# Optimization experiments

Hardware: AMD Instinct MI355X
Metric: run time of the kernel (lower is better)

## Reference

```python
import jax, jax.numpy as jnp
import numpy as np

B, N, FEAT, HID, CTX = 16384, 7, 512, 256, 256
COMB = N * HID + CTX  # 2048


def setup_inputs() -> dict:
    key = jax.random.key(0)
    ks = jax.random.split(key, 20)
    s = lambda k, shape, sc=0.05: jax.random.normal(k, shape, dtype=jnp.float32) * sc
    adj = jax.random.randint(ks[1], (N, N), 0, 2).astype(jnp.float32)
    # guarantee self-loops so no row is fully masked (still exercise nan_to_num path robustly)
    adj = jnp.maximum(adj, jnp.eye(N, dtype=jnp.float32))
    return {
        "node_feats": jax.random.normal(ks[0], (B, N, FEAT), dtype=jnp.float32),
        "adj": adj,
        "context": jax.random.normal(ks[2], (B, CTX), dtype=jnp.float32),
        "base_preds": jax.random.normal(ks[3], (B, 5), dtype=jnp.float32),
        "W1": s(ks[4], (HID, FEAT)),
        "a1": s(ks[5], (1, 2 * HID)),
        "W2": s(ks[6], (HID, HID)),
        "a2": s(ks[7], (1, 2 * HID)),
        "wh1_w": s(ks[8], (32, COMB)), "wh1_b": s(ks[9], (32,)),
        "wh2_w": s(ks[10], (16, 32)), "wh2_b": s(ks[11], (16,)),
        "wh3_w": s(ks[12], (5, 16)), "wh3_b": s(ks[13], (5,)),
        "rh1_w": s(ks[14], (16, COMB)), "rh1_b": s(ks[15], (16,)),
        "rh2_w": s(ks[16], (1, 16)), "rh2_b": s(ks[17], (1,)),
    }


def _gat_layer(x, adj, W, a):
    # x: (B, N, in_dim); W: (D, in_dim); a: (1, 2D)
    h = jnp.einsum('bni,di->bnd', x, W)  # (B, N, D)
    D = W.shape[0]
    # a([h_i, h_j]) == h_i @ a[:, :D] + h_j @ a[:, D:]
    s_i = h @ a[0, :D]   # (B, N)
    s_j = h @ a[0, D:]   # (B, N)
    e = s_i[:, :, None] + s_j[:, None, :]          # (B, N, N)
    e = jax.nn.leaky_relu(e, negative_slope=0.2)
    e = jnp.where(adj[None] == 0, -jnp.inf, e)
    alpha = jax.nn.softmax(e, axis=-1)
    alpha = jnp.nan_to_num(alpha, nan=0.0)
    out = jnp.einsum('bij,bjd->bid', alpha, h)     # (B, N, D)
    return out, alpha


def reference(node_feats, adj, context, base_preds, W1, a1, W2, a2,
              wh1_w, wh1_b, wh2_w, wh2_b, wh3_w, wh3_b,
              rh1_w, rh1_b, rh2_w, rh2_b):
    h, _attn1 = _gat_layer(node_feats, adj, W1, a1)
    h = jax.nn.relu(h)
    h, attn2 = _gat_layer(h, adj, W2, a2)
    h = jax.nn.relu(h)
    graph_embed = h.reshape(h.shape[0], -1)                 # (B, N*D)
    combined = jnp.concatenate([graph_embed, context], -1)  # (B, COMB)
    # weight head (dropout is inference-mode identity)
    t = jax.nn.relu(combined @ wh1_w.T + wh1_b)
    t = jax.nn.relu(t @ wh2_w.T + wh2_b)
    raw_weights = t @ wh3_w.T + wh3_b                       # (B, 5)
    weights = jax.nn.softmax(raw_weights, axis=-1)
    weighted_pred = jnp.sum(weights * base_preds, axis=-1)  # (B,)
    r = jnp.tanh(combined @ rh1_w.T + rh1_b)
    residual = (r @ rh2_w.T + rh2_b)[:, 0] * 0.05
    pred = jnp.maximum(weighted_pred + residual, 0.05)
    return pred, weights, attn2
```

## Files before the change

### kernel.cpp

```cpp
#include <hip/hip_runtime.h>

#define B_SZ 16384
#define NN 7
#define HID 256
#define CTXD 256
#define COMB 2048

typedef __attribute__((ext_vector_type(8))) short short8;
typedef __attribute__((ext_vector_type(4))) float floatx4;
typedef __attribute__((ext_vector_type(4))) unsigned short ushortx4;

__device__ __forceinline__ float bf2f(unsigned short u) {
    union { unsigned int i; float f; } v; v.i = ((unsigned int)u) << 16; return v.f;
}
__device__ __forceinline__ unsigned short f2bf(float f) {
    union { unsigned int i; float f; } v; v.f = f;
    return (unsigned short)((v.i + 0x7FFFu + ((v.i >> 16) & 1u)) >> 16);
}
__device__ __forceinline__ unsigned short f2bf_fast(float f) {
    union { unsigned int i; float f; } v; v.f = f;
    return (unsigned short)((v.i + 0x8000u) >> 16);
}

__device__ __forceinline__ void gl_lds16(const unsigned short* g, unsigned short* l) {
    __builtin_amdgcn_global_load_lds(
        (const __attribute__((address_space(1))) unsigned int*)g,
        (__attribute__((address_space(3))) unsigned int*)l, 16, 0, 0);
}

__global__ __launch_bounds__(256) void cvt_bf16(const float* __restrict__ s,
                                                unsigned short* __restrict__ d, int n) {
    int i = (blockIdx.x * 256 + threadIdx.x) * 4;
    if (i >= n) return;
    floatx4 v = *(const floatx4*)(s + i);
    ushortx4 o = {f2bf(v[0]), f2bf(v[1]), f2bf(v[2]), f2bf(v[3])};
    *(ushortx4*)(d + i) = o;
}

template <bool AFP32>
__global__ __launch_bounds__(256) void gemm128(const void* __restrict__ Ap,
                                               const unsigned short* __restrict__ Wb,
                                               unsigned short* __restrict__ C,
                                               int nb, int K) {
    __shared__ __attribute__((aligned(16))) unsigned short As[128 * 32];
    __shared__ __attribute__((aligned(16))) unsigned short Bs[128 * 32];
    const int tid = threadIdx.x;
    const long rowBase = (long)(blockIdx.x / nb) * 128;
    const int colBase = (blockIdx.x % nb) * 128;
    const int N = nb * 128;
    const int wave = tid >> 6, lane = tid & 63;
    const int wm = wave >> 1, wn = wave & 1;
    const int quad = lane >> 4, m16 = lane & 15;
    const int srow = tid >> 2, scol = (tid & 3) * 8;

    floatx4 acc[4][4];
#pragma unroll
    for (int mt = 0; mt < 4; ++mt)
#pragma unroll
        for (int nt = 0; nt < 4; ++nt) acc[mt][nt] = (floatx4){0.f, 0.f, 0.f, 0.f};

    const unsigned short* Ab = (const unsigned short*)Ap;
    const float* Af = (const float*)Ap;

    for (int k0 = 0; k0 < K; k0 += 32) {
        if constexpr (AFP32) {
            const int r = tid >> 1, c = (tid & 1) * 16;
            const floatx4* src = (const floatx4*)(Af + (rowBase + r) * (long)K + k0 + c);
            floatx4 v0 = src[0], v1 = src[1], v2 = src[2], v3 = src[3];
            short8 s0, s1;
            s0[0] = f2bf_fast(v0[0]); s0[1] = f2bf_fast(v0[1]);
            s0[2] = f2bf_fast(v0[2]); s0[3] = f2bf_fast(v0[3]);
            s0[4] = f2bf_fast(v1[0]); s0[5] = f2bf_fast(v1[1]);
            s0[6] = f2bf_fast(v1[2]); s0[7] = f2bf_fast(v1[3]);
            s1[0] = f2bf_fast(v2[0]); s1[1] = f2bf_fast(v2[1]);
            s1[2] = f2bf_fast(v2[2]); s1[3] = f2bf_fast(v2[3]);
            s1[4] = f2bf_fast(v3[0]); s1[5] = f2bf_fast(v3[1]);
            s1[6] = f2bf_fast(v3[2]); s1[7] = f2bf_fast(v3[3]);
            *(short8*)&As[r * 32 + c] = s0;
            *(short8*)&As[r * 32 + c + 8] = s1;
        } else {
            gl_lds16(Ab + (rowBase + srow) * (long)K + k0 + scol, &As[wave * 512]);
            gl_lds16(Ab + (rowBase + 64 + srow) * (long)K + k0 + scol, &As[2048 + wave * 512]);
        }
        gl_lds16(Wb + (long)(colBase + srow) * K + k0 + scol, &Bs[wave * 512]);
        gl_lds16(Wb + (long)(colBase + 64 + srow) * K + k0 + scol, &Bs[2048 + wave * 512]);
        __syncthreads();
        short8 af[4], bfr[4];
#pragma unroll
        for (int t = 0; t < 4; ++t)
            af[t] = *(const short8*)&As[(wm * 64 + t * 16 + m16) * 32 + quad * 8];
#pragma unroll
        for (int t = 0; t < 4; ++t)
            bfr[t] = *(const short8*)&Bs[(wn * 64 + t * 16 + m16) * 32 + quad * 8];
#pragma unroll
        for (int mt = 0; mt < 4; ++mt)
#pragma unroll
            for (int nt = 0; nt < 4; ++nt)
                acc[mt][nt] = __builtin_amdgcn_mfma_f32_16x16x32_bf16(af[mt], bfr[nt], acc[mt][nt], 0, 0, 0);
        __syncthreads();
    }
#pragma unroll
    for (int mt = 0; mt < 4; ++mt)
#pragma unroll
        for (int nt = 0; nt < 4; ++nt)
#pragma unroll
            for (int i = 0; i < 4; ++i) {
                long m = rowBase + wm * 64 + mt * 16 + quad * 4 + i;
                int n = colBase + wn * 64 + nt * 16 + m16;
                C[m * (long)N + n] = f2bf(acc[mt][nt][i]);
            }
}

template <int OUTSTRIDE, bool WRITE_ALPHA, bool COPY_CTX>
__global__ __launch_bounds__(256) void attn_v2(const unsigned short* __restrict__ h,
                                               const float* __restrict__ adj,
                                               const float* __restrict__ avec,
                                               unsigned short* __restrict__ outb,
                                               float* __restrict__ alpha_out,
                                               const float* __restrict__ context) {
    __shared__ float adjs[NN * NN];
    const int tid = threadIdx.x, wave = tid >> 6, lane = tid & 63;
    if (tid < NN * NN) adjs[tid] = adj[tid];
    __syncthreads();
    const long b = (long)blockIdx.x * 4 + wave;
    const unsigned short* hb = h + b * (NN * HID);

    float hv[NN][4];
#pragma unroll
    for (int n = 0; n < NN; ++n) {
        ushortx4 r = *(const ushortx4*)(hb + n * HID + lane * 4);
        hv[n][0] = bf2f(r[0]); hv[n][1] = bf2f(r[1]);
        hv[n][2] = bf2f(r[2]); hv[n][3] = bf2f(r[3]);
    }
    floatx4 ai = *(const floatx4*)(avec + lane * 4);
    floatx4 aj = *(const floatx4*)(avec + HID + lane * 4);

    float si[NN], sj[NN];
#pragma unroll
    for (int n = 0; n < NN; ++n) {
        float pi = hv[n][0] * ai[0] + hv[n][1] * ai[1] + hv[n][2] * ai[2] + hv[n][3] * ai[3];
        float pj = hv[n][0] * aj[0] + hv[n][1] * aj[1] + hv[n][2] * aj[2] + hv[n][3] * aj[3];
#pragma unroll
        for (int off = 32; off; off >>= 1) {
            pi += __shfl_xor(pi, off);
            pj += __shfl_xor(pj, off);
        }
        si[n] = pi; sj[n] = pj;
    }
    const int j = lane & 7;
    float sjm = sj[0];
    if (j == 1) sjm = sj[1];
    if (j == 2) sjm = sj[2];
    if (j == 3) sjm = sj[3];
    if (j == 4) sjm = sj[4];
    if (j == 5) sjm = sj[5];
    if (j == 6) sjm = sj[6];
    const int jc = (j < 7) ? j : 0;

    float alpha[NN];
#pragma unroll
    for (int i = 0; i < NN; ++i) {
        float x = si[i] + sjm;
        x = (x >= 0.f) ? x : 0.2f * x;
        bool ok = (j < 7) && (adjs[i * 7 + jc] != 0.f);
        float e = ok ? x : -1e30f;
        float m = e;
        m = fmaxf(m, __shfl_xor(m, 1, 8));
        m = fmaxf(m, __shfl_xor(m, 2, 8));
        m = fmaxf(m, __shfl_xor(m, 4, 8));
        float ex = ok ? __expf(e - m) : 0.f;
        float s = ex;
        s += __shfl_xor(s, 1, 8);
        s += __shfl_xor(s, 2, 8);
        s += __shfl_xor(s, 4, 8);
        alpha[i] = (s > 0.f) ? ex * __frcp_rn(s) : 0.f;
    }
    if (WRITE_ALPHA && lane < 7) {
#pragma unroll
        for (int i = 0; i < NN; ++i)
            alpha_out[b * (NN * NN) + i * NN + lane] = alpha[i];
    }
    unsigned short* ob = outb + b * OUTSTRIDE;
#pragma unroll
    for (int i = 0; i < NN; ++i) {
        floatx4 o = (floatx4){0.f, 0.f, 0.f, 0.f};
#pragma unroll
        for (int jj = 0; jj < NN; ++jj) {
            float a = __shfl(alpha[i], jj, 8);
            o[0] += a * hv[jj][0]; o[1] += a * hv[jj][1];
            o[2] += a * hv[jj][2]; o[3] += a * hv[jj][3];
        }
        ushortx4 st = {f2bf(fmaxf(o[0], 0.f)), f2bf(fmaxf(o[1], 0.f)),
                       f2bf(fmaxf(o[2], 0.f)), f2bf(fmaxf(o[3], 0.f))};
        *(ushortx4*)(ob + i * HID + lane * 4) = st;
    }
    if (COPY_CTX) {
        floatx4 c = *(const floatx4*)(context + b * CTXD + lane * 4);
        ushortx4 st = {f2bf(c[0]), f2bf(c[1]), f2bf(c[2]), f2bf(c[3])};
        *(ushortx4*)(ob + NN * HID + lane * 4) = st;
    }
}

__global__ __launch_bounds__(256) void head_gemm(const unsigned short* __restrict__ A,
                                                 const unsigned short* __restrict__ Wb,
                                                 float* __restrict__ outp) {
    __shared__ __attribute__((aligned(16))) unsigned short As[64][40];
    __shared__ __attribute__((aligned(16))) unsigned short Bs[48][40];
    const int tid = threadIdx.x;
    const long rowBase = (long)blockIdx.x * 64;
    const int ks = blockIdx.y;
    const int wave = tid >> 6, lane = tid & 63;
    const int quad = lane >> 4, m16 = lane & 15;
    floatx4 acc[3];
#pragma unroll
    for (int t = 0; t < 3; ++t) acc[t] = (floatx4){0.f, 0.f, 0.f, 0.f};
    const int kBeg = ks * 512;
    for (int k0 = kBeg; k0 < kBeg + 512; k0 += 32) {
        {
            int r = tid >> 2, c = (tid & 3) * 8;
            *(short8*)&As[r][c] = *(const short8*)(A + (rowBase + r) * (long)COMB + k0 + c);
        }
        if (tid < 192) {
            int r = tid >> 2, c = (tid & 3) * 8;
            *(short8*)&Bs[r][c] = *(const short8*)(Wb + r * (long)COMB + k0 + c);
        }
        __syncthreads();
        short8 a = *(const short8*)&As[wave * 16 + m16][quad * 8];
#pragma unroll
        for (int t = 0; t < 3; ++t) {
            short8 bfr = *(const short8*)&Bs[t * 16 + m16][quad * 8];
            acc[t] = __builtin_amdgcn_mfma_f32_16x16x32_bf16(a, bfr, acc[t], 0, 0, 0);
        }
        __syncthreads();
    }
    float* op = outp + (long)ks * B_SZ * 48;
#pragma unroll
    for (int t = 0; t < 3; ++t)
#pragma unroll
        for (int i = 0; i < 4; ++i) {
            long m = rowBase + wave * 16 + quad * 4 + i;
            op[m * 48 + t * 16 + m16] = acc[t][i];
        }
}

__global__ __launch_bounds__(256) void head_finalize(const float* __restrict__ rawp,
                                                     const float* __restrict__ wh1_b,
                                                     const float* __restrict__ wh2_w,
                                                     const float* __restrict__ wh2_b,
                                                     const float* __restrict__ wh3_w,
                                                     const float* __restrict__ wh3_b,
                                                     const float* __restrict__ rh1_b,
                                                     const float* __restrict__ rh2_w,
                                                     const float* __restrict__ rh2_b,
                                                     const float* __restrict__ base_preds,
                                                     float* __restrict__ out) {
    const int b = blockIdx.x * 256 + threadIdx.x;
    const size_t P = (size_t)B_SZ * 48;
    const float* g0 = rawp + (long)b * 48;
    float t1[32], r1[16];
#pragma unroll
    for (int k = 0; k < 32; ++k) {
        float g = g0[k] + g0[P + k] + g0[2 * P + k] + g0[3 * P + k];
        t1[k] = fmaxf(g + wh1_b[k], 0.f);
    }
#pragma unroll
    for (int k = 0; k < 16; ++k) {
        float g = g0[32 + k] + g0[P + 32 + k] + g0[2 * P + 32 + k] + g0[3 * P + 32 + k];
        r1[k] = tanhf(g + rh1_b[k]);
    }
    float t2[16];
#pragma unroll
    for (int jj = 0; jj < 16; ++jj) {
        float s = wh2_b[jj];
        for (int k = 0; k < 32; ++k) s += wh2_w[jj * 32 + k] * t1[k];
        t2[jj] = fmaxf(s, 0.f);
    }
    float rw[5], m = -1e30f;
#pragma unroll
    for (int o = 0; o < 5; ++o) {
        float s = wh3_b[o];
        for (int jj = 0; jj < 16; ++jj) s += wh3_w[o * 16 + jj] * t2[jj];
        rw[o] = s; m = fmaxf(m, s);
    }
    float se = 0.f;
#pragma unroll
    for (int o = 0; o < 5; ++o) { rw[o] = __expf(rw[o] - m); se += rw[o]; }
    float inv = 1.f / se, wp = 0.f;
#pragma unroll
    for (int o = 0; o < 5; ++o) {
        float w = rw[o] * inv;
        out[B_SZ + (long)b * 5 + o] = w;
        wp += w * base_preds[(long)b * 5 + o];
    }
    float rs = rh2_b[0];
#pragma unroll
    for (int k = 0; k < 16; ++k) rs += rh2_w[k] * r1[k];
    out[b] = fmaxf(wp + rs * 0.05f, 0.05f);
}

extern "C" void kernel_launch(void* const* d_in, const int* in_sizes, int n_in,
                              void* d_out, int out_size, void* d_ws, size_t ws_size,
                              hipStream_t stream) {
    const float* node_feats = (const float*)d_in[0];
    const float* adj        = (const float*)d_in[1];
    const float* context    = (const float*)d_in[2];
    const float* base_preds = (const float*)d_in[3];
    const float* W1         = (const float*)d_in[4];
    const float* a1         = (const float*)d_in[5];
    const float* W2         = (const float*)d_in[6];
    const float* a2         = (const float*)d_in[7];
    const float* wh1_w = (const float*)d_in[8];
    const float* wh1_b = (const float*)d_in[9];
    const float* wh2_w = (const float*)d_in[10];
    const float* wh2_b = (const float*)d_in[11];
    const float* wh3_w = (const float*)d_in[12];
    const float* wh3_b = (const float*)d_in[13];
    const float* rh1_w = (const float*)d_in[14];
    const float* rh1_b = (const float*)d_in[15];
    const float* rh2_w = (const float*)d_in[16];
    const float* rh2_b = (const float*)d_in[17];
    float* out = (float*)d_out;

    char* ws = (char*)d_ws;
    const size_t HB = (size_t)B_SZ * NN * HID * 2;
    unsigned short* h1       = (unsigned short*)ws;
    unsigned short* x2       = (unsigned short*)(ws + HB);
    unsigned short* h2pre    = h1;
    unsigned short* combined = (unsigned short*)(ws + 2 * HB);
    float* rawp = (float*)(ws + HB);
    unsigned short* W1b = (unsigned short*)(ws + 2 * HB + (size_t)B_SZ * COMB * 2);
    unsigned short* W2b = W1b + 256 * 512;
    unsigned short* Whb = W2b + 256 * 256;

    const int M1 = B_SZ * NN;

    cvt_bf16<<<128, 256, 0, stream>>>(W1, W1b, 256 * 512);
    cvt_bf16<<<64, 256, 0, stream>>>(W2, W2b, 256 * 256);
    cvt_bf16<<<64, 256, 0, stream>>>(wh1_w, Whb, 32 * 2048);
    cvt_bf16<<<32, 256, 0, stream>>>(rh1_w, Whb + 32 * 2048, 16 * 2048);

    gemm128<true><<<(M1 / 128) * 2, 256, 0, stream>>>(node_feats, W1b, h1, 2, 512);

    attn_v2<NN * HID, false, false><<<B_SZ / 4, 256, 0, stream>>>(h1, adj, a1, x2, nullptr, nullptr);

    gemm128<false><<<(M1 / 128) * 2, 256, 0, stream>>>(x2, W2b, h2pre, 2, 256);

    attn_v2<COMB, true, true><<<B_SZ / 4, 256, 0, stream>>>(h2pre, adj, a2, combined,
                                                            out + 6 * B_SZ, context);

    head_gemm<<<dim3(B_SZ / 64, 4), 256, 0, stream>>>(combined, Whb, rawp);

    head_finalize<<<B_SZ / 256, 256, 0, stream>>>(rawp, wh1_b, wh2_w, wh2_b, wh3_w, wh3_b,
                                                  rh1_b, rh2_w, rh2_b, base_preds, out);
}
```

Measured before the change: 572.3 us.

## Fuse GAT layers, attention and heads into two kernels with graph-aligned tiles

Replaces the pipeline of separate GEMM, attention, head GEMM and finalize kernels with two fused kernels. Each block handles 16 graphs (112 rows) against all 256 output columns, so attention runs directly on the LDS tile. The second kernel also computes both head projections and the final softmax/prediction in-block, and the four weight-conversion launches become one. This removes intermediate h/combined/partial-sum round trips through global memory and several launches, at the cost of large LDS use (~81KB and ~119KB per block), lower occupancy, and 7x2 MFMA tiles per wave.

```diff
diff --git a/kernel.cpp b/kernel.cpp
--- a/kernel.cpp
+++ b/kernel.cpp
@@ -3,138 +3,59 @@
 #define B_SZ 16384
 #define NN 7
 #define HID 256
-#define CTXD 256
 #define COMB 2048
 
 typedef __attribute__((ext_vector_type(8))) short short8;
 typedef __attribute__((ext_vector_type(4))) float floatx4;
 typedef __attribute__((ext_vector_type(4))) unsigned short ushortx4;
-
-__device__ __forceinline__ float bf2f(unsigned short u) {
+typedef unsigned short us;
+
+__device__ __forceinline__ float bf2f(us u) {
     union { unsigned int i; float f; } v; v.i = ((unsigned int)u) << 16; return v.f;
 }
-__device__ __forceinline__ unsigned short f2bf(float f) {
+__device__ __forceinline__ us f2bf(float f) {
     union { unsigned int i; float f; } v; v.f = f;
-    return (unsigned short)((v.i + 0x7FFFu + ((v.i >> 16) & 1u)) >> 16);
-}
-__device__ __forceinline__ unsigned short f2bf_fast(float f) {
+    return (us)((v.i + 0x7FFFu + ((v.i >> 16) & 1u)) >> 16);
+}
+__device__ __forceinline__ us f2bf_fast(float f) {
     union { unsigned int i; float f; } v; v.f = f;
-    return (unsigned short)((v.i + 0x8000u) >> 16);
-}
-
-__device__ __forceinline__ void gl_lds16(const unsigned short* g, unsigned short* l) {
+    return (us)((v.i + 0x8000u) >> 16);
+}
+__device__ __forceinline__ void gl_lds16(const us* g, us* l) {
     __builtin_amdgcn_global_load_lds(
         (const __attribute__((address_space(1))) unsigned int*)g,
         (__attribute__((address_space(3))) unsigned int*)l, 16, 0, 0);
 }
 
-__global__ __launch_bounds__(256) void cvt_bf16(const float* __restrict__ s,
-                                                unsigned short* __restrict__ d, int n) {
+__global__ __launch_bounds__(256) void pack_weights(const float* __restrict__ W1,
+                                                    const float* __restrict__ W2,
+                                                    const float* __restrict__ wh1,
+                                                    const float* __restrict__ rh1,
+                                                    us* __restrict__ dst) {
     int i = (blockIdx.x * 256 + threadIdx.x) * 4;
-    if (i >= n) return;
-    floatx4 v = *(const floatx4*)(s + i);
+    if (i >= 294912) return;
+    const float* src; int off;
+    if (i < 131072)      { src = W1;  off = i; }
+    else if (i < 196608) { src = W2;  off = i - 131072; }
+    else if (i < 262144) { src = wh1; off = i - 196608; }
+    else                 { src = rh1; off = i - 262144; }
+    floatx4 v = *(const floatx4*)(src + off);
     ushortx4 o = {f2bf(v[0]), f2bf(v[1]), f2bf(v[2]), f2bf(v[3])};
-    *(ushortx4*)(d + i) = o;
-}
-
-template <bool AFP32>
-__global__ __launch_bounds__(256) void gemm128(const void* __restrict__ Ap,
-                                               const unsigned short* __restrict__ Wb,
-                                               unsigned short* __restrict__ C,
-                                               int nb, int K) {
-    __shared__ __attribute__((aligned(16))) unsigned short As[128 * 32];
-    __shared__ __attribute__((aligned(16))) unsigned short Bs[128 * 32];
-    const int tid = threadIdx.x;
-    const long rowBase = (long)(blockIdx.x / nb) * 128;
-    const int colBase = (blockIdx.x % nb) * 128;
-    const int N = nb * 128;
-    const int wave = tid >> 6, lane = tid & 63;
-    const int wm = wave >> 1, wn = wave & 1;
-    const int quad = lane >> 4, m16 = lane & 15;
-    const int srow = tid >> 2, scol = (tid & 3) * 8;
-
-    floatx4 acc[4][4];
-#pragma unroll
-    for (int mt = 0; mt < 4; ++mt)
-#pragma unroll
-        for (int nt = 0; nt < 4; ++nt) acc[mt][nt] = (floatx4){0.f, 0.f, 0.f, 0.f};
-
-    const unsigned short* Ab = (const unsigned short*)Ap;
-    const float* Af = (const float*)Ap;
-
-    for (int k0 = 0; k0 < K; k0 += 32) {
-        if constexpr (AFP32) {
-            const int r = tid >> 1, c = (tid & 1) * 16;
-            const floatx4* src = (const floatx4*)(Af + (rowBase + r) * (long)K + k0 + c);
-            floatx4 v0 = src[0], v1 = src[1], v2 = src[2], v3 = src[3];
-            short8 s0, s1;
-            s0[0] = f2bf_fast(v0[0]); s0[1] = f2bf_fast(v0[1]);
-            s0[2] = f2bf_fast(v0[2]); s0[3] = f2bf_fast(v0[3]);
-            s0[4] = f2bf_fast(v1[0]); s0[5] = f2bf_fast(v1[1]);
-            s0[6] = f2bf_fast(v1[2]); s0[7] = f2bf_fast(v1[3]);
-            s1[0] = f2bf_fast(v2[0]); s1[1] = f2bf_fast(v2[1]);
-            s1[2] = f2bf_fast(v2[2]); s1[3] = f2bf_fast(v2[3]);
-            s1[4] = f2bf_fast(v3[0]); s1[5] = f2bf_fast(v3[1]);
-            s1[6] = f2bf_fast(v3[2]); s1[7] = f2bf_fast(v3[3]);
-            *(short8*)&As[r * 32 + c] = s0;
-            *(short8*)&As[r * 32 + c + 8] = s1;
-        } else {
-            gl_lds16(Ab + (rowBase + srow) * (long)K + k0 + scol, &As[wave * 512]);
-            gl_lds16(Ab + (rowBase + 64 + srow) * (long)K + k0 + scol, &As[2048 + wave * 512]);
-        }
-        gl_lds16(Wb + (long)(colBase + srow) * K + k0 + scol, &Bs[wave * 512]);
-        gl_lds16(Wb + (long)(colBase + 64 + srow) * K + k0 + scol, &Bs[2048 + wave * 512]);
-        __syncthreads();
-        short8 af[4], bfr[4];
-#pragma unroll
-        for (int t = 0; t < 4; ++t)
-            af[t] = *(const short8*)&As[(wm * 64 + t * 16 + m16) * 32 + quad * 8];
-#pragma unroll
-        for (int t = 0; t < 4; ++t)
-            bfr[t] = *(const short8*)&Bs[(wn * 64 + t * 16 + m16) * 32 + quad * 8];
-#pragma unroll
-        for (int mt = 0; mt < 4; ++mt)
-#pragma unroll
-            for (int nt = 0; nt < 4; ++nt)
-                acc[mt][nt] = __builtin_amdgcn_mfma_f32_16x16x32_bf16(af[mt], bfr[nt], acc[mt][nt], 0, 0, 0);
-        __syncthreads();
-    }
-#pragma unroll
-    for (int mt = 0; mt < 4; ++mt)
-#pragma unroll
-        for (int nt = 0; nt < 4; ++nt)
-#pragma unroll
-            for (int i = 0; i < 4; ++i) {
-                long m = rowBase + wm * 64 + mt * 16 + quad * 4 + i;
-                int n = colBase + wn * 64 + nt * 16 + m16;
-                C[m * (long)N + n] = f2bf(acc[mt][nt][i]);
-            }
-}
-
-template <int OUTSTRIDE, bool WRITE_ALPHA, bool COPY_CTX>
-__global__ __launch_bounds__(256) void attn_v2(const unsigned short* __restrict__ h,
-                                               const float* __restrict__ adj,
-                                               const float* __restrict__ avec,
-                                               unsigned short* __restrict__ outb,
-                                               float* __restrict__ alpha_out,
-                                               const float* __restrict__ context) {
-    __shared__ float adjs[NN * NN];
-    const int tid = threadIdx.x, wave = tid >> 6, lane = tid & 63;
-    if (tid < NN * NN) adjs[tid] = adj[tid];
-    __syncthreads();
-    const long b = (long)blockIdx.x * 4 + wave;
-    const unsigned short* hb = h + b * (NN * HID);
-
+    *(ushortx4*)(dst + i) = o;
+}
+
+template <int SRC_STRIDE, bool WRITE_ALPHA>
+__device__ __forceinline__ void attn_graph(const us* hb, const float* adjs, const float* avec,
+                                           us* dst, int dstStride, float* alpha_dst, int lane) {
     float hv[NN][4];
 #pragma unroll
     for (int n = 0; n < NN; ++n) {
-        ushortx4 r = *(const ushortx4*)(hb + n * HID + lane * 4);
+        ushortx4 r = *(const ushortx4*)(hb + n * SRC_STRIDE + lane * 4);
         hv[n][0] = bf2f(r[0]); hv[n][1] = bf2f(r[1]);
         hv[n][2] = bf2f(r[2]); hv[n][3] = bf2f(r[3]);
     }
     floatx4 ai = *(const floatx4*)(avec + lane * 4);
     floatx4 aj = *(const floatx4*)(avec + HID + lane * 4);
-
     float si[NN], sj[NN];
 #pragma unroll
     for (int n = 0; n < NN; ++n) {
@@ -156,7 +77,6 @@
     if (j == 5) sjm = sj[5];
     if (j == 6) sjm = sj[6];
     const int jc = (j < 7) ? j : 0;
-
     float alpha[NN];
 #pragma unroll
     for (int i = 0; i < NN; ++i) {
@@ -177,10 +97,8 @@
     }
     if (WRITE_ALPHA && lane < 7) {
 #pragma unroll
-        for (int i = 0; i < NN; ++i)
-            alpha_out[b * (NN * NN) + i * NN + lane] = alpha[i];
-    }
-    unsigned short* ob = outb + b * OUTSTRIDE;
+        for (int i = 0; i < NN; ++i) alpha_dst[i * NN + lane] = alpha[i];
+    }
 #pragma unroll
     for (int i = 0; i < NN; ++i) {
         floatx4 o = (floatx4){0.f, 0.f, 0.f, 0.f};
@@ -192,110 +110,242 @@
         }
         ushortx4 st = {f2bf(fmaxf(o[0], 0.f)), f2bf(fmaxf(o[1], 0.f)),
                        f2bf(fmaxf(o[2], 0.f)), f2bf(fmaxf(o[3], 0.f))};
-        *(ushortx4*)(ob + i * HID + lane * 4) = st;
-    }
-    if (COPY_CTX) {
-        floatx4 c = *(const floatx4*)(context + b * CTXD + lane * 4);
-        ushortx4 st = {f2bf(c[0]), f2bf(c[1]), f2bf(c[2]), f2bf(c[3])};
-        *(ushortx4*)(ob + NN * HID + lane * 4) = st;
-    }
-}
-
-__global__ __launch_bounds__(256) void head_gemm(const unsigned short* __restrict__ A,
-                                                 const unsigned short* __restrict__ Wb,
-                                                 float* __restrict__ outp) {
-    __shared__ __attribute__((aligned(16))) unsigned short As[64][40];
-    __shared__ __attribute__((aligned(16))) unsigned short Bs[48][40];
+        *(ushortx4*)(dst + i * dstStride + lane * 4) = st;
+    }
+}
+
+__global__ __launch_bounds__(512) void fused_g1(const float* __restrict__ Af,
+                                                const us* __restrict__ W1b,
+                                                const float* __restrict__ adj,
+                                                const float* __restrict__ avec,
+                                                us* __restrict__ x2g) {
+    extern __shared__ __attribute__((aligned(16))) char smem[];
+    us* As = (us*)smem;
+    us* Bs = (us*)(smem + 7168);
+    us* hs = (us*)(smem + 23552);
+    float* adjs = (float*)(smem + 80896);
+
     const int tid = threadIdx.x;
-    const long rowBase = (long)blockIdx.x * 64;
-    const int ks = blockIdx.y;
     const int wave = tid >> 6, lane = tid & 63;
     const int quad = lane >> 4, m16 = lane & 15;
-    floatx4 acc[3];
-#pragma unroll
-    for (int t = 0; t < 3; ++t) acc[t] = (floatx4){0.f, 0.f, 0.f, 0.f};
-    const int kBeg = ks * 512;
-    for (int k0 = kBeg; k0 < kBeg + 512; k0 += 32) {
+    const long rowBase = (long)blockIdx.x * 112;
+    if (tid < 49) adjs[tid] = adj[tid];
+
+    floatx4 acc[7][2];
+#pragma unroll
+    for (int rt = 0; rt < 7; ++rt)
+#pragma unroll
+        for (int ct = 0; ct < 2; ++ct) acc[rt][ct] = (floatx4){0.f, 0.f, 0.f, 0.f};
+
+    for (int k0 = 0; k0 < 512; k0 += 32) {
+        if (tid < 448) {
+            int r = tid >> 2, kh = tid & 3;
+            const floatx4* src = (const floatx4*)(Af + (rowBase + r) * 512 + k0 + kh * 8);
+            floatx4 v0 = src[0], v1 = src[1];
+            short8 s;
+            s[0] = f2bf_fast(v0[0]); s[1] = f2bf_fast(v0[1]);
+            s[2] = f2bf_fast(v0[2]); s[3] = f2bf_fast(v0[3]);
+            s[4] = f2bf_fast(v1[0]); s[5] = f2bf_fast(v1[1]);
+            s[6] = f2bf_fast(v1[2]); s[7] = f2bf_fast(v1[3]);
+            *(short8*)&As[(r >> 4) * 512 + (kh * 16 + (r & 15)) * 8] = s;
+        }
         {
-            int r = tid >> 2, c = (tid & 3) * 8;
-            *(short8*)&As[r][c] = *(const short8*)(A + (rowBase + r) * (long)COMB + k0 + c);
-        }
-        if (tid < 192) {
-            int r = tid >> 2, c = (tid & 3) * 8;
-            *(short8*)&Bs[r][c] = *(const short8*)(Wb + r * (long)COMB + k0 + c);
+            int b1 = wave * 16, b2 = 128 + wave * 16;
+            gl_lds16(W1b + (long)(b1 + (lane & 15)) * 512 + k0 + (lane >> 4) * 8, &Bs[b1 * 32]);
+            gl_lds16(W1b + (long)(b2 + (lane & 15)) * 512 + k0 + (lane >> 4) * 8, &Bs[b2 * 32]);
         }
         __syncthreads();
-        short8 a = *(const short8*)&As[wave * 16 + m16][quad * 8];
-#pragma unroll
-        for (int t = 0; t < 3; ++t) {
-            short8 bfr = *(const short8*)&Bs[t * 16 + m16][quad * 8];
-            acc[t] = __builtin_amdgcn_mfma_f32_16x16x32_bf16(a, bfr, acc[t], 0, 0, 0);
-        }
+        short8 af[7], bf[2];
+#pragma unroll
+        for (int rt = 0; rt < 7; ++rt)
+            af[rt] = *(const short8*)&As[rt * 512 + (quad * 16 + m16) * 8];
+#pragma unroll
+        for (int ct = 0; ct < 2; ++ct)
+            bf[ct] = *(const short8*)&Bs[(wave * 2 + ct) * 512 + (quad * 16 + m16) * 8];
+#pragma unroll
+        for (int rt = 0; rt < 7; ++rt)
+#pragma unroll
+            for (int ct = 0; ct < 2; ++ct)
+                acc[rt][ct] = __builtin_amdgcn_mfma_f32_16x16x32_bf16(af[rt], bf[ct], acc[rt][ct], 0, 0, 0);
         __syncthreads();
     }
-    float* op = outp + (long)ks * B_SZ * 48;
-#pragma unroll
-    for (int t = 0; t < 3; ++t)
-#pragma unroll
-        for (int i = 0; i < 4; ++i) {
-            long m = rowBase + wave * 16 + quad * 4 + i;
-            op[m * 48 + t * 16 + m16] = acc[t][i];
-        }
-}
-
-__global__ __launch_bounds__(256) void head_finalize(const float* __restrict__ rawp,
-                                                     const float* __restrict__ wh1_b,
-                                                     const float* __restrict__ wh2_w,
-                                                     const float* __restrict__ wh2_b,
-                                                     const float* __restrict__ wh3_w,
-                                                     const float* __restrict__ wh3_b,
-                                                     const float* __restrict__ rh1_b,
-                                                     const float* __restrict__ rh2_w,
-                                                     const float* __restrict__ rh2_b,
-                                                     const float* __restrict__ base_preds,
-                                                     float* __restrict__ out) {
-    const int b = blockIdx.x * 256 + threadIdx.x;
-    const size_t P = (size_t)B_SZ * 48;
-    const float* g0 = rawp + (long)b * 48;
-    float t1[32], r1[16];
-#pragma unroll
-    for (int k = 0; k < 32; ++k) {
-        float g = g0[k] + g0[P + k] + g0[2 * P + k] + g0[3 * P + k];
-        t1[k] = fmaxf(g + wh1_b[k], 0.f);
-    }
-#pragma unroll
-    for (int k = 0; k < 16; ++k) {
-        float g = g0[32 + k] + g0[P + 32 + k] + g0[2 * P + 32 + k] + g0[3 * P + 32 + k];
-        r1[k] = tanhf(g + rh1_b[k]);
-    }
-    float t2[16];
-#pragma unroll
-    for (int jj = 0; jj < 16; ++jj) {
-        float s = wh2_b[jj];
-        for (int k = 0; k < 32; ++k) s += wh2_w[jj * 32 + k] * t1[k];
-        t2[jj] = fmaxf(s, 0.f);
-    }
-    float rw[5], m = -1e30f;
-#pragma unroll
-    for (int o = 0; o < 5; ++o) {
-        float s = wh3_b[o];
-        for (int jj = 0; jj < 16; ++jj) s += wh3_w[o * 16 + jj] * t2[jj];
-        rw[o] = s; m = fmaxf(m, s);
-    }
-    float se = 0.f;
-#pragma unroll
-    for (int o = 0; o < 5; ++o) { rw[o] = __expf(rw[o] - m); se += rw[o]; }
-    float inv = 1.f / se, wp = 0.f;
-#pragma unroll
-    for (int o = 0; o < 5; ++o) {
-        float w = rw[o] * inv;
-        out[B_SZ + (long)b * 5 + o] = w;
-        wp += w * base_preds[(long)b * 5 + o];
-    }
-    float rs = rh2_b[0];
-#pragma unroll
-    for (int k = 0; k < 16; ++k) rs += rh2_w[k] * r1[k];
-    out[b] = fmaxf(wp + rs * 0.05f, 0.05f);
+#pragma unroll
+    for (int rt = 0; rt < 7; ++rt)
+#pragma unroll
+        for (int ct = 0; ct < 2; ++ct)
+#pragma unroll
+            for (int i = 0; i < 4; ++i)
+                hs[(rt * 16 + quad * 4 + i) * 256 + wave * 32 + ct * 16 + m16] = f2bf(acc[rt][ct][i]);
+    __syncthreads();
+#pragma unroll
+    for (int gg = 0; gg < 2; ++gg) {
+        int gl = wave * 2 + gg;
+        long b = (long)blockIdx.x * 16 + gl;
+        attn_graph<256, false>(&hs[gl * 7 * 256], adjs, avec,
+                               x2g + b * 7 * 256, 256, nullptr, lane);
+    }
+}
+
+__global__ __launch_bounds__(512) void fused_rest(const us* __restrict__ x2g,
+                                                  const us* __restrict__ W2b,
+                                                  const us* __restrict__ Whb,
+                                                  const float* __restrict__ adj,
+                                                  const float* __restrict__ avec,
+                                                  const float* __restrict__ context,
+                                                  const float* __restrict__ wh1_b,
+                                                  const float* __restrict__ wh2_w,
+                                                  const float* __restrict__ wh2_b,
+                                                  const float* __restrict__ wh3_w,
+                                                  const float* __restrict__ wh3_b,
+                                                  const float* __restrict__ rh1_b,
+                                                  const float* __restrict__ rh2_w,
+                                                  const float* __restrict__ rh2_b,
+                                                  const float* __restrict__ base_preds,
+                                                  float* __restrict__ out) {
+    extern __shared__ __attribute__((aligned(16))) char smem[];
+    us* As = (us*)smem;
+    us* Bs = (us*)(smem + 8192);
+    us* hs = (us*)(smem + 24576);
+    us* ctxs = (us*)(smem + 82816);
+    float* red = (float*)(smem + 91136);
+    float* fin = (float*)(smem + 115712);
+    float* adjs = (float*)(smem + 118784);
+
+    const int tid = threadIdx.x;
+    const int wave = tid >> 6, lane = tid & 63;
+    const int quad = lane >> 4, m16 = lane & 15;
+    const long rowBase = (long)blockIdx.x * 112;
+    const long gbase = (long)blockIdx.x * 16;
+    if (tid < 49) adjs[tid] = adj[tid];
+    {
+        int r = tid >> 5, c = (tid & 31) * 8;
+        const floatx4* src = (const floatx4*)(context + (gbase + r) * 256 + c);
+        floatx4 v0 = src[0], v1 = src[1];
+        short8 s;
+        s[0] = f2bf(v0[0]); s[1] = f2bf(v0[1]); s[2] = f2bf(v0[2]); s[3] = f2bf(v0[3]);
+        s[4] = f2bf(v1[0]); s[5] = f2bf(v1[1]); s[6] = f2bf(v1[2]); s[7] = f2bf(v1[3]);
+        *(short8*)&ctxs[r * 260 + c] = s;
+    }
+
+    floatx4 acc[7][2];
+#pragma unroll
+    for (int rt = 0; rt < 7; ++rt)
+#pragma unroll
+        for (int ct = 0; ct < 2; ++ct) acc[rt][ct] = (floatx4){0.f, 0.f, 0.f, 0.f};
+
+    for (int k0 = 0; k0 < 256; k0 += 32) {
+        gl_lds16(x2g + (rowBase + wave * 16 + (lane & 15)) * 256 + k0 + (lane >> 4) * 8,
+                 &As[wave * 512]);
+        {
+            int b1 = wave * 16, b2 = 128 + wave * 16;
+            gl_lds16(W2b + (long)(b1 + (lane & 15)) * 256 + k0 + (lane >> 4) * 8, &Bs[b1 * 32]);
+            gl_lds16(W2b + (long)(b2 + (lane & 15)) * 256 + k0 + (lane >> 4) * 8, &Bs[b2 * 32]);
+        }
+        __syncthreads();
+        short8 af[7], bf[2];
+#pragma unroll
+        for (int rt = 0; rt < 7; ++rt)
+            af[rt] = *(const short8*)&As[rt * 512 + (quad * 16 + m16) * 8];
+#pragma unroll
+        for (int ct = 0; ct < 2; ++ct)
+            bf[ct] = *(const short8*)&Bs[(wave * 2 + ct) * 512 + (quad * 16 + m16) * 8];
+#pragma unroll
+        for (int rt = 0; rt < 7; ++rt)
+#pragma unroll
+            for (int ct = 0; ct < 2; ++ct)
+                acc[rt][ct] = __builtin_amdgcn_mfma_f32_16x16x32_bf16(af[rt], bf[ct], acc[rt][ct], 0, 0, 0);
+        __syncthreads();
+    }
+#pragma unroll
+    for (int rt = 0; rt < 7; ++rt)
+#pragma unroll
+        for (int ct = 0; ct < 2; ++ct)
+#pragma unroll
+            for (int i = 0; i < 4; ++i)
+                hs[(rt * 16 + quad * 4 + i) * 260 + wave * 32 + ct * 16 + m16] = f2bf(acc[rt][ct][i]);
+    __syncthreads();
+    float* alf = out + 6 * B_SZ;
+#pragma unroll
+    for (int gg = 0; gg < 2; ++gg) {
+        int gl = wave * 2 + gg;
+        long b = gbase + gl;
+        attn_graph<260, true>(&hs[gl * 7 * 260], adjs, avec,
+                              &hs[gl * 7 * 260], 260, alf + b * 49, lane);
+    }
+    __syncthreads();
+    floatx4 acc3[3];
+#pragma unroll
+    for (int ct = 0; ct < 3; ++ct) acc3[ct] = (floatx4){0.f, 0.f, 0.f, 0.f};
+    const long wk = (long)wave * 256;
+#pragma unroll
+    for (int s = 0; s < 8; ++s) {
+        int kk = s * 32;
+        short8 a;
+        if (wave < 7) a = *(const short8*)&hs[(m16 * 7 + wave) * 260 + kk + quad * 8];
+        else          a = *(const short8*)&ctxs[m16 * 260 + kk + quad * 8];
+#pragma unroll
+        for (int ct = 0; ct < 3; ++ct) {
+            short8 bh = *(const short8*)(Whb + (long)(ct * 16 + m16) * COMB + wk + kk + quad * 8);
+            acc3[ct] = __builtin_amdgcn_mfma_f32_16x16x32_bf16(a, bh, acc3[ct], 0, 0, 0);
+        }
+    }
+#pragma unroll
+    for (int ct = 0; ct < 3; ++ct)
+#pragma unroll
+        for (int i = 0; i < 4; ++i)
+            red[wave * 768 + (quad * 4 + i) * 48 + ct * 16 + m16] = acc3[ct][i];
+    __syncthreads();
+    {
+        float s = 0.f;
+#pragma unroll
+        for (int w = 0; w < 8; ++w) s += red[w * 768 + tid];
+        fin[tid] = s;
+        if (tid < 256) {
+            float s2 = 0.f;
+#pragma unroll
+            for (int w = 0; w < 8; ++w) s2 += red[w * 768 + 512 + tid];
+            fin[512 + tid] = s2;
+        }
+    }
+    __syncthreads();
+    if (tid < 16) {
+        const int g = tid;
+        const long b = gbase + g;
+        const float* g48 = &fin[g * 48];
+        float t1[32], r1[16];
+#pragma unroll
+        for (int k = 0; k < 32; ++k) t1[k] = fmaxf(g48[k] + wh1_b[k], 0.f);
+#pragma unroll
+        for (int k = 0; k < 16; ++k) r1[k] = tanhf(g48[32 + k] + rh1_b[k]);
+        float t2[16];
+#pragma unroll
+        for (int jj = 0; jj < 16; ++jj) {
+            float s = wh2_b[jj];
+            for (int k = 0; k < 32; ++k) s += wh2_w[jj * 32 + k] * t1[k];
+            t2[jj] = fmaxf(s, 0.f);
+        }
+        float rw[5], m = -1e30f;
+#pragma unroll
+        for (int o = 0; o < 5; ++o) {
+            float s = wh3_b[o];
+            for (int jj = 0; jj < 16; ++jj) s += wh3_w[o * 16 + jj] * t2[jj];
+            rw[o] = s; m = fmaxf(m, s);
+        }
+        float se = 0.f;
+#pragma unroll
+        for (int o = 0; o < 5; ++o) { rw[o] = __expf(rw[o] - m); se += rw[o]; }
+        float inv = 1.f / se, wp = 0.f;
+#pragma unroll
+        for (int o = 0; o < 5; ++o) {
+            float w = rw[o] * inv;
+            out[B_SZ + b * 5 + o] = w;
+            wp += w * base_preds[b * 5 + o];
+        }
+        float rs = rh2_b[0];
+#pragma unroll
+        for (int k = 0; k < 16; ++k) rs += rh2_w[k] * r1[k];
+        out[b] = fmaxf(wp + rs * 0.05f, 0.05f);
+    }
 }
 
 extern "C" void kernel_launch(void* const* d_in, const int* in_sizes, int n_in,
@@ -323,33 +373,16 @@
 
     char* ws = (char*)d_ws;
     const size_t HB = (size_t)B_SZ * NN * HID * 2;
-    unsigned short* h1       = (unsigned short*)ws;
-    unsigned short* x2       = (unsigned short*)(ws + HB);
-    unsigned short* h2pre    = h1;
-    unsigned short* combined = (unsigned short*)(ws + 2 * HB);
-    float* rawp = (float*)(ws + HB);
-    unsigned short* W1b = (unsigned short*)(ws + 2 * HB + (size_t)B_SZ * COMB * 2);
-    unsigned short* W2b = W1b + 256 * 512;
-    unsigned short* Whb = W2b + 256 * 256;
-
-    const int M1 = B_SZ * NN;
-
-    cvt_bf16<<<128, 256, 0, stream>>>(W1, W1b, 256 * 512);
-    cvt_bf16<<<64, 256, 0, stream>>>(W2, W2b, 256 * 256);
-    cvt_bf16<<<64, 256, 0, stream>>>(wh1_w, Whb, 32 * 2048);
-    cvt_bf16<<<32, 256, 0, stream>>>(rh1_w, Whb + 32 * 2048, 16 * 2048);
-
-    gemm128<true><<<(M1 / 128) * 2, 256, 0, stream>>>(node_feats, W1b, h1, 2, 512);
-
-    attn_v2<NN * HID, false, false><<<B_SZ / 4, 256, 0, stream>>>(h1, adj, a1, x2, nullptr, nullptr);
-
-    gemm128<false><<<(M1 / 128) * 2, 256, 0, stream>>>(x2, W2b, h2pre, 2, 256);
-
-    attn_v2<COMB, true, true><<<B_SZ / 4, 256, 0, stream>>>(h2pre, adj, a2, combined,
-                                                            out + 6 * B_SZ, context);
-
-    head_gemm<<<dim3(B_SZ / 64, 4), 256, 0, stream>>>(combined, Whb, rawp);
-
-    head_finalize<<<B_SZ / 256, 256, 0, stream>>>(rawp, wh1_b, wh2_w, wh2_b, wh3_w, wh3_b,
-                                                  rh1_b, rh2_w, rh2_b, base_preds, out);
-}
+    us* x2  = (us*)ws;
+    us* W1b = (us*)(ws + HB);
+    us* W2b = W1b + 131072;
+    us* Whb = W2b + 65536;
+
+    pack_weights<<<288, 256, 0, stream>>>(W1, W2, wh1_w, rh1_w, W1b);
+
+    fused_g1<<<1024, 512, 81104, stream>>>(node_feats, W1b, adj, a1, x2);
+
+    fused_rest<<<1024, 512, 118992, stream>>>(x2, W2b, Whb, adj, a2, context,
+                                              wh1_b, wh2_w, wh2_b, wh3_w, wh3_b,
+                                              rh1_b, rh2_w, rh2_b, base_preds, out);
+}
```

Result: faster. 541.7 us (-5.3%).
